# Kernel tuning notes

Measured on AMD Instinct MI355X. Metric: run time of the kernel, lower is better.

## Reference

```python
import jax, jax.numpy as jnp
import numpy as np

EPS = 1e-5
SCALE_MIN, SCALE_MAX = 0.6, 1.0


def _layer_norm(x):
    m = jnp.mean(x, axis=-1, keepdims=True)
    v = jnp.mean((x - m) ** 2, axis=-1, keepdims=True)
    return (x - m) / jnp.sqrt(v + EPS)


def _scan_dir(seq, A, Bp, Cp, D, W_in, W_out, snr_scale):
    """seq: [B, L, C] -> [B, L, C]. Diagonal SSM recurrence h = A*h + B*u."""
    Bsz, L, C = seq.shape
    N = A.shape[0]
    seq = _layer_norm(seq)
    u = jnp.einsum('blc,nc->bln', seq, W_in)                 # input_proj, [B,L,N]
    A_base = jnp.tanh(A)[None, :]                            # [1,N]
    s = jnp.clip(snr_scale, 0.0, 1.0)[:, None]               # [B,1]
    scale = SCALE_MIN + (SCALE_MAX - SCALE_MIN) * s
    Ad = jnp.clip(A_base * scale, -0.99, 0.99)               # [B,N]
    Bu = Bp[None, None, :] * u                               # [B,L,N]

    def step(h, bu_t):
        h = Ad * h + bu_t
        return h, h

    h0 = jnp.zeros((Bsz, N), dtype=seq.dtype)
    _, hs = jax.lax.scan(step, h0, jnp.swapaxes(Bu, 0, 1))   # hs: [L,B,N]
    hs = jnp.swapaxes(hs, 0, 1)                              # [B,L,N]
    y_state = Cp[None, None, :] * hs
    y = jnp.einsum('bln,cn->blc', y_state, W_out)            # output_proj
    return y + D[None, None, :] * seq


def _forward(x, snr_scale, A, Bparam, Cparam, D, W_in, W_out):
    Bsz, H, W, C = x.shape
    L = H * W
    if L > 4000:
        x = _layer_norm(x)
    # row scans
    seq_row = x.reshape(Bsz, L, C)
    y_row_f = _scan_dir(seq_row, A, Bparam, Cparam, D, W_in, W_out, snr_scale)
    y_row_b = _scan_dir(seq_row[:, ::-1, :], A, Bparam, Cparam, D, W_in, W_out, snr_scale)
    y_row = 0.5 * (y_row_f + y_row_b[:, ::-1, :])
    y_row = y_row.reshape(Bsz, H, W, C)
    # column scans
    x_col = jnp.transpose(x, (0, 2, 1, 3))                   # [B,W,H,C]
    seq_col = x_col.reshape(Bsz, L, C)
    y_col_f = _scan_dir(seq_col, A, Bparam, Cparam, D, W_in, W_out, snr_scale)
    y_col_b = _scan_dir(seq_col[:, ::-1, :], A, Bparam, Cparam, D, W_in, W_out, snr_scale)
    y_col = 0.5 * (y_col_f + y_col_b[:, ::-1, :])
    y_col = jnp.transpose(y_col.reshape(Bsz, W, H, C), (0, 2, 1, 3))
    return 0.5 * (y_row + y_col)


def setup_inputs() -> dict:
    key = jax.random.key(0)
    k = jax.random.split(key, 4)
    Bsz, H, W, C, N = 8, 64, 64, 256, 64
    x = jax.random.normal(k[0], (Bsz, H, W, C), dtype=jnp.float32)
    snr_scale = jax.random.uniform(k[1], (Bsz,), dtype=jnp.float32)
    A = -0.5 * jnp.ones((N,), dtype=jnp.float32)
    Bparam = 0.5 * jnp.ones((N,), dtype=jnp.float32)
    Cparam = 0.5 * jnp.ones((N,), dtype=jnp.float32)
    D = jnp.zeros((C,), dtype=jnp.float32)
    # nn.Linear default init: U(-1/sqrt(fan_in), 1/sqrt(fan_in))
    W_in = jax.random.uniform(k[2], (N, C), dtype=jnp.float32,
                              minval=-1.0 / np.sqrt(C), maxval=1.0 / np.sqrt(C))
    W_out = jax.random.uniform(k[3], (C, N), dtype=jnp.float32,
                               minval=-1.0 / np.sqrt(N), maxval=1.0 / np.sqrt(N))
    return {"x": x, "snr_scale": snr_scale, "A": A, "Bparam": Bparam,
            "Cparam": Cparam, "D": D, "W_in": W_in, "W_out": W_out}


def reference(x, snr_scale, A, Bparam, Cparam, D, W_in, W_out):
    return _forward(x, snr_scale, A, Bparam, Cparam, D, W_in, W_out)
```

## Files before the change

kernel.cpp:

```cpp
#include <hip/hip_runtime.h>
#include <hip/hip_bf16.h>
#include <math.h>

#define Bsz 8
#define Hh 64
#define Ww 64
#define Cc 256
#define Nn 64
#define Ll 4096
#define EPSf 1e-5f

typedef __bf16 v8bf __attribute__((ext_vector_type(8)));
typedef float  f32x4 __attribute__((ext_vector_type(4)));

__device__ __forceinline__ float ad_val(float a, float snr) {
    float s = fminf(fmaxf(snr, 0.f), 1.f);
    float scale = 0.6f + 0.4f * s;
    float v = tanhf(a) * scale;
    return fminf(fmaxf(v, -0.99f), 0.99f);
}

__global__ __launch_bounds__(256) void k0_weights(
    const float* __restrict__ Win, const float* __restrict__ Wout,
    const float* __restrict__ Bp, __bf16* __restrict__ Wh,
    __bf16* __restrict__ Wl, __bf16* __restrict__ Wo, float* __restrict__ WB)
{
    const int t = threadIdx.x;
    for (int idx = t; idx < 32 * 64; idx += 256) {
        int tile = idx >> 6, lane = idx & 63;
        int kt = tile >> 2, nt = tile & 3;
        int q = lane >> 4, n = nt * 16 + (lane & 15);
        #pragma unroll
        for (int j = 0; j < 8; ++j) {
            int k = kt * 32 + q * 8 + j;
            float w = Win[n * Cc + k];
            __bf16 h = (__bf16)w;
            Wh[idx * 8 + j] = h;
            Wl[idx * 8 + j] = (__bf16)(w - (float)h);
        }
    }
    for (int idx = t; idx < 32 * 64; idx += 256) {
        int tile = idx >> 6, lane = idx & 63;
        int kt = tile >> 4, ntg = tile & 15;
        int q = lane >> 4, c = ntg * 16 + (lane & 15);
        #pragma unroll
        for (int j = 0; j < 8; ++j) {
            int k = kt * 32 + q * 8 + j;
            Wo[idx * 8 + j] = (__bf16)Wout[c * Nn + k];
        }
    }
    if (t < 64) {
        float s = 0.f;
        for (int c2 = 0; c2 < Cc; ++c2) s += Win[t * Cc + c2];
        WB[t] = s * Bp[t];
    }
}

__global__ __launch_bounds__(256) void k1_ln_gemm(
    const float* __restrict__ x, const __bf16* __restrict__ Wh,
    const __bf16* __restrict__ Wl, const float* __restrict__ Bp,
    const float* __restrict__ WB, float* __restrict__ Bu,
    float* __restrict__ Mst, float* __restrict__ Sst)
{
    __shared__ float mrow[64], srow[64];
    const int t = threadIdx.x;
    const int lane = t & 63;
    const int wv = __builtin_amdgcn_readfirstlane(t >> 6);
    const long pbase = (long)blockIdx.x * 64;
    const float* xt = x + pbase * Cc;

    for (int rr = 0; rr < 16; ++rr) {
        int r = wv * 16 + rr;
        float4 v = ((const float4*)(xt + (long)r * Cc))[lane];
        float s = v.x + v.y + v.z + v.w;
        float q = v.x*v.x + v.y*v.y + v.z*v.z + v.w*v.w;
        #pragma unroll
        for (int off = 32; off > 0; off >>= 1) {
            s += __shfl_down(s, off);
            q += __shfl_down(q, off);
        }
        if (lane == 0) {
            float m = s * (1.f/256.f);
            float var = fmaxf(q * (1.f/256.f) - m*m, 0.f);
            float r1 = rsqrtf(var + EPSf);
            float v2 = var / (var + EPSf);
            float sc = r1 * rsqrtf(v2 + EPSf);
            mrow[r] = m;
            srow[r] = sc;
            Mst[pbase + r] = m;
            Sst[pbase + r] = sc;
        }
    }
    __syncthreads();

    const int q = lane >> 4;
    const int mi = lane & 15;
    const float* xa = xt + (long)(wv * 16 + mi) * Cc + q * 8;

    f32x4 acc[4];
    #pragma unroll
    for (int nt = 0; nt < 4; ++nt) acc[nt] = (f32x4){0.f, 0.f, 0.f, 0.f};

    #pragma unroll
    for (int kt = 0; kt < 8; ++kt) {
        float4 a0 = *(const float4*)(xa + kt * 32);
        float4 a1 = *(const float4*)(xa + kt * 32 + 4);
        float av[8] = {a0.x, a0.y, a0.z, a0.w, a1.x, a1.y, a1.z, a1.w};
        v8bf ah, al;
        #pragma unroll
        for (int j = 0; j < 8; ++j) {
            __bf16 h = (__bf16)av[j];
            ah[j] = h;
            al[j] = (__bf16)(av[j] - (float)h);
        }
        #pragma unroll
        for (int nt = 0; nt < 4; ++nt) {
            v8bf bh = *(const v8bf*)(Wh + ((long)(kt * 4 + nt) * 64 + lane) * 8);
            v8bf bl = *(const v8bf*)(Wl + ((long)(kt * 4 + nt) * 64 + lane) * 8);
            acc[nt] = __builtin_amdgcn_mfma_f32_16x16x32_bf16(ah, bh, acc[nt], 0, 0, 0);
            acc[nt] = __builtin_amdgcn_mfma_f32_16x16x32_bf16(al, bh, acc[nt], 0, 0, 0);
            acc[nt] = __builtin_amdgcn_mfma_f32_16x16x32_bf16(ah, bl, acc[nt], 0, 0, 0);
        }
    }

    #pragma unroll
    for (int nt = 0; nt < 4; ++nt) {
        int n = nt * 16 + mi;
        float bpn = Bp[n];
        float wbn = WB[n];
        #pragma unroll
        for (int reg = 0; reg < 4; ++reg) {
            int p = wv * 16 + q * 4 + reg;
            float m = mrow[p], s = srow[p];
            Bu[(pbase + p) * Nn + n] = s * (acc[nt][reg] * bpn - m * wbn);
        }
    }
}

__global__ __launch_bounds__(64) void k2_carry(
    const float* __restrict__ Bu, const float* __restrict__ A,
    const float* __restrict__ snr, float* __restrict__ E)
{
    __shared__ float tile[64 * 65];
    const int lane = threadIdx.x;
    const int id = blockIdx.x;
    const int isCol = id >> 9;
    const int b = (id >> 6) & 7;
    const int j = id & 63;
    const float Ad = ad_val(A[lane], snr[b]);
    const float* src = Bu + ((long)b * Ll + (isCol ? j : j * 64)) * Nn;
    const long stride = isCol ? (long)Ww * Nn : Nn;
    for (int k = 0; k < 64; ++k)
        tile[k * 65 + lane] = src[k * stride + lane];
    __syncthreads();
    float s = 0.f;
    #pragma unroll 8
    for (int k = 0; k < 64; ++k) s = fmaf(Ad, s, tile[k * 65 + lane]);
    const int dF = isCol ? 2 : 0;
    E[((dF * 8 + b) * 64 + j) * 64 + lane] = s;
    s = 0.f;
    #pragma unroll 8
    for (int k = 63; k >= 0; --k) s = fmaf(Ad, s, tile[k * 65 + lane]);
    E[(((dF + 1) * 8 + b) * 64 + (63 - j)) * 64 + lane] = s;
}

__global__ __launch_bounds__(64) void k3_scan_carries(
    const float* __restrict__ E, float* __restrict__ Hx,
    const float* __restrict__ A, const float* __restrict__ snr)
{
    const int lane = threadIdx.x;
    const int db = blockIdx.x;
    const int b = db & 7;
    float Ad = ad_val(A[lane], snr[b]);
    float p = Ad;
    #pragma unroll
    for (int i = 0; i < 6; ++i) p *= p;
    float s = 0.f;
    const float* e = E + (long)db * 64 * 64;
    float* h = Hx + (long)db * 64 * 64;
    for (int jj = 0; jj < 64; ++jj) {
        h[jj * 64 + lane] = s;
        s = fmaf(p, s, e[jj * 64 + lane]);
    }
}

__global__ __launch_bounds__(64) void k4_apply(
    const float* __restrict__ Bu, const float* __restrict__ Hx,
    const float* __restrict__ A, const float* __restrict__ snr,
    const float* __restrict__ Cp, float* __restrict__ Srow,
    float* __restrict__ Scol)
{
    __shared__ float tile[64 * 65];
    __shared__ float hf[64 * 65];
    const int lane = threadIdx.x;
    const int id = blockIdx.x;
    const int isCol = id >> 9;
    const int b = (id >> 6) & 7;
    const int j = id & 63;
    const float Ad = ad_val(A[lane], snr[b]);
    const float cp = 0.25f * Cp[lane];
    const float* src = Bu + ((long)b * Ll + (isCol ? j : j * 64)) * Nn;
    const long stride = isCol ? (long)Ww * Nn : Nn;
    for (int k = 0; k < 64; ++k)
        tile[k * 65 + lane] = src[k * stride + lane];
    __syncthreads();
    const int dF = isCol ? 2 : 0;
    float s = Hx[((dF * 8 + b) * 64 + j) * 64 + lane];
    for (int k = 0; k < 64; ++k) {
        s = fmaf(Ad, s, tile[k * 65 + lane]);
        hf[k * 65 + lane] = s;
    }
    float sb = Hx[(((dF + 1) * 8 + b) * 64 + (63 - j)) * 64 + lane];
    float* out0 = (isCol ? Scol : Srow) + ((long)b * Ll + (isCol ? j : j * 64)) * Nn;
    for (int k = 63; k >= 0; --k) {
        sb = fmaf(Ad, sb, tile[k * 65 + lane]);
        out0[k * stride + lane] = cp * (sb + hf[k * 65 + lane]);
    }
}

__global__ __launch_bounds__(256) void k5_gemm_out(
    const float* __restrict__ Srow, const float* __restrict__ Scol,
    const float* __restrict__ x, const __bf16* __restrict__ Wo,
    const float* __restrict__ Dp, const float* __restrict__ Mst,
    const float* __restrict__ Sst, float* __restrict__ out)
{
    const int t = threadIdx.x;
    const int lane = t & 63;
    const int wv = __builtin_amdgcn_readfirstlane(t >> 6);
    const int mtile = wv >> 1;
    const int nh = wv & 1;
    const long pbase = (long)blockIdx.x * 32;
    const int q = lane >> 4;
    const int mi = lane & 15;

    const float* sr = Srow + (pbase + mtile * 16 + mi) * Nn + q * 8;
    const float* sc = Scol + (pbase + mtile * 16 + mi) * Nn + q * 8;

    f32x4 acc[8];
    #pragma unroll
    for (int nt = 0; nt < 8; ++nt) acc[nt] = (f32x4){0.f, 0.f, 0.f, 0.f};

    #pragma unroll
    for (int kt = 0; kt < 2; ++kt) {
        float4 r0 = *(const float4*)(sr + kt * 32);
        float4 r1 = *(const float4*)(sr + kt * 32 + 4);
        float4 c0 = *(const float4*)(sc + kt * 32);
        float4 c1 = *(const float4*)(sc + kt * 32 + 4);
        float sv[8] = {r0.x + c0.x, r0.y + c0.y, r0.z + c0.z, r0.w + c0.w,
                       r1.x + c1.x, r1.y + c1.y, r1.z + c1.z, r1.w + c1.w};
        v8bf af;
        #pragma unroll
        for (int j = 0; j < 8; ++j) af[j] = (__bf16)sv[j];
        #pragma unroll
        for (int nt = 0; nt < 8; ++nt) {
            int ntg = nh * 8 + nt;
            v8bf b = *(const v8bf*)(Wo + ((long)(kt * 16 + ntg) * 64 + lane) * 8);
            acc[nt] = __builtin_amdgcn_mfma_f32_16x16x32_bf16(af, b, acc[nt], 0, 0, 0);
        }
    }

    #pragma unroll
    for (int nt = 0; nt < 8; ++nt) {
        int c = nh * 128 + nt * 16 + mi;
        float dc = Dp[c];
        #pragma unroll
        for (int reg = 0; reg < 4; ++reg) {
            long p = pbase + mtile * 16 + q * 4 + reg;
            float m = Mst[p], s = Sst[p];
            long off = p * Cc + c;
            out[off] = acc[nt][reg] + dc * ((x[off] - m) * s);
        }
    }
}

extern "C" void kernel_launch(void* const* d_in, const int* in_sizes, int n_in,
                              void* d_out, int out_size, void* d_ws, size_t ws_size,
                              hipStream_t stream)
{
    const float* x    = (const float*)d_in[0];
    const float* snr  = (const float*)d_in[1];
    const float* A    = (const float*)d_in[2];
    const float* Bp   = (const float*)d_in[3];
    const float* Cp   = (const float*)d_in[4];
    const float* Dp   = (const float*)d_in[5];
    const float* Win  = (const float*)d_in[6];
    const float* Wout = (const float*)d_in[7];
    float* out = (float*)d_out;

    char* ws = (char*)d_ws;
    float*  Bu   = (float*)(ws);
    float*  Srow = (float*)(ws + (size_t)8  * 1024 * 1024);
    float*  Scol = (float*)(ws + (size_t)16 * 1024 * 1024);
    float*  E    = (float*)(ws + (size_t)24 * 1024 * 1024);
    float*  Hx   = (float*)(ws + (size_t)24 * 1024 * 1024 + 512*1024);
    float*  Mst  = (float*)(ws + (size_t)25 * 1024 * 1024);
    float*  Sst  = (float*)(ws + (size_t)25 * 1024 * 1024 + 128*1024);
    char*   wbase = ws + (size_t)25 * 1024 * 1024 + 512 * 1024;
    __bf16* Wh   = (__bf16*)(wbase);
    __bf16* Wl   = (__bf16*)(wbase + 32 * 1024);
    __bf16* Wo   = (__bf16*)(wbase + 64 * 1024);
    float*  WB   = (float*)(wbase + 96 * 1024);

    hipLaunchKernelGGL(k0_weights,      dim3(1),    dim3(256), 0, stream, Win, Wout, Bp, Wh, Wl, Wo, WB);
    hipLaunchKernelGGL(k1_ln_gemm,      dim3(512),  dim3(256), 0, stream, x, Wh, Wl, Bp, WB, Bu, Mst, Sst);
    hipLaunchKernelGGL(k2_carry,        dim3(1024), dim3(64),  0, stream, Bu, A, snr, E);
    hipLaunchKernelGGL(k3_scan_carries, dim3(32),   dim3(64),  0, stream, E, Hx, A, snr);
    hipLaunchKernelGGL(k4_apply,        dim3(1024), dim3(64),  0, stream, Bu, Hx, A, snr, Cp, Srow, Scol);
    hipLaunchKernelGGL(k5_gemm_out,     dim3(1024), dim3(256), 0, stream, Srow, Scol, x, Wo, Dp, Mst, Sst, out);
}
```

Measured before the change: 155.6 us.

## Fuse scan stages into cooperative kernel and stage GEMM tiles through shared memory

```diff
diff --git a/kernel.cpp b/kernel.cpp
--- a/kernel.cpp
+++ b/kernel.cpp
@@ -1,6 +1,9 @@
 #include <hip/hip_runtime.h>
 #include <hip/hip_bf16.h>
+#include <hip/hip_cooperative_groups.h>
 #include <math.h>
+
+namespace cg = cooperative_groups;
 
 #define Bsz 8
 #define Hh 64
@@ -20,39 +23,53 @@
     return fminf(fmaxf(v, -0.99f), 0.99f);
 }
 
+__device__ __forceinline__ v8bf cvt8(float4 a, float4 b) {
+    v8bf r;
+    r[0] = (__bf16)a.x; r[1] = (__bf16)a.y; r[2] = (__bf16)a.z; r[3] = (__bf16)a.w;
+    r[4] = (__bf16)b.x; r[5] = (__bf16)b.y; r[6] = (__bf16)b.z; r[7] = (__bf16)b.w;
+    return r;
+}
+
 __global__ __launch_bounds__(256) void k0_weights(
     const float* __restrict__ Win, const float* __restrict__ Wout,
     const float* __restrict__ Bp, __bf16* __restrict__ Wh,
     __bf16* __restrict__ Wl, __bf16* __restrict__ Wo, float* __restrict__ WB)
 {
     const int t = threadIdx.x;
-    for (int idx = t; idx < 32 * 64; idx += 256) {
-        int tile = idx >> 6, lane = idx & 63;
-        int kt = tile >> 2, nt = tile & 3;
-        int q = lane >> 4, n = nt * 16 + (lane & 15);
-        #pragma unroll
-        for (int j = 0; j < 8; ++j) {
-            int k = kt * 32 + q * 8 + j;
-            float w = Win[n * Cc + k];
-            __bf16 h = (__bf16)w;
-            Wh[idx * 8 + j] = h;
-            Wl[idx * 8 + j] = (__bf16)(w - (float)h);
-        }
-    }
-    for (int idx = t; idx < 32 * 64; idx += 256) {
-        int tile = idx >> 6, lane = idx & 63;
-        int kt = tile >> 4, ntg = tile & 15;
-        int q = lane >> 4, c = ntg * 16 + (lane & 15);
-        #pragma unroll
-        for (int j = 0; j < 8; ++j) {
-            int k = kt * 32 + q * 8 + j;
-            Wo[idx * 8 + j] = (__bf16)Wout[c * Nn + k];
-        }
-    }
-    if (t < 64) {
+    const int blk = blockIdx.x;
+    if (blk < 4) {
+        for (int idx = blk * 512 + t; idx < blk * 512 + 512; idx += 256) {
+            int tile = idx >> 6, lane = idx & 63;
+            int kt = tile >> 2, nt = tile & 3;
+            int q = lane >> 4, n = nt * 16 + (lane & 15);
+            #pragma unroll
+            for (int j = 0; j < 8; ++j) {
+                int k = kt * 32 + q * 8 + j;
+                float w = Win[n * Cc + k];
+                __bf16 h = (__bf16)w;
+                Wh[idx * 8 + j] = h;
+                Wl[idx * 8 + j] = (__bf16)(w - (float)h);
+            }
+        }
+    } else if (blk < 8) {
+        for (int idx = (blk - 4) * 512 + t; idx < (blk - 4) * 512 + 512; idx += 256) {
+            int tile = idx >> 6, lane = idx & 63;
+            int kt = tile >> 4, ntg = tile & 15;
+            int q = lane >> 4, c = ntg * 16 + (lane & 15);
+            #pragma unroll
+            for (int j = 0; j < 8; ++j)
+                Wo[idx * 8 + j] = (__bf16)Wout[c * Nn + kt * 32 + q * 8 + j];
+        }
+    } else {
+        __shared__ float wtmp[256];
+        int n = t >> 2, qd = t & 3;
         float s = 0.f;
-        for (int c2 = 0; c2 < Cc; ++c2) s += Win[t * Cc + c2];
-        WB[t] = s * Bp[t];
+        const float* wr = Win + (long)n * Cc + qd * 64;
+        for (int i = 0; i < 64; ++i) s += wr[i];
+        wtmp[t] = s;
+        __syncthreads();
+        if (t < 64)
+            WB[t] = (wtmp[t*4] + wtmp[t*4+1] + wtmp[t*4+2] + wtmp[t*4+3]) * Bp[t];
     }
 }
 
@@ -62,16 +79,18 @@
     const float* __restrict__ WB, float* __restrict__ Bu,
     float* __restrict__ Mst, float* __restrict__ Sst)
 {
+    __shared__ float xs[64 * 260];
     __shared__ float mrow[64], srow[64];
     const int t = threadIdx.x;
     const int lane = t & 63;
     const int wv = __builtin_amdgcn_readfirstlane(t >> 6);
     const long pbase = (long)blockIdx.x * 64;
-    const float* xt = x + pbase * Cc;
-
-    for (int rr = 0; rr < 16; ++rr) {
-        int r = wv * 16 + rr;
-        float4 v = ((const float4*)(xt + (long)r * Cc))[lane];
+    const float4* xg = (const float4*)(x + pbase * Cc);
+
+    for (int i = 0; i < 16; ++i) {
+        int r = i * 4 + wv;
+        float4 v = xg[i * 256 + t];
+        *(float4*)&xs[r * 260 + lane * 4] = v;
         float s = v.x + v.y + v.z + v.w;
         float q = v.x*v.x + v.y*v.y + v.z*v.z + v.w*v.w;
         #pragma unroll
@@ -85,17 +104,14 @@
             float r1 = rsqrtf(var + EPSf);
             float v2 = var / (var + EPSf);
             float sc = r1 * rsqrtf(v2 + EPSf);
-            mrow[r] = m;
-            srow[r] = sc;
-            Mst[pbase + r] = m;
-            Sst[pbase + r] = sc;
+            mrow[r] = m; srow[r] = sc;
+            Mst[pbase + r] = m; Sst[pbase + r] = sc;
         }
     }
     __syncthreads();
 
     const int q = lane >> 4;
     const int mi = lane & 15;
-    const float* xa = xt + (long)(wv * 16 + mi) * Cc + q * 8;
 
     f32x4 acc[4];
     #pragma unroll
@@ -103,8 +119,9 @@
 
     #pragma unroll
     for (int kt = 0; kt < 8; ++kt) {
-        float4 a0 = *(const float4*)(xa + kt * 32);
-        float4 a1 = *(const float4*)(xa + kt * 32 + 4);
+        const float* ar = &xs[(wv * 16 + mi) * 260 + q * 8 + kt * 32];
+        float4 a0 = *(const float4*)ar;
+        float4 a1 = *(const float4*)(ar + 4);
         float av[8] = {a0.x, a0.y, a0.z, a0.w, a1.x, a1.y, a1.z, a1.w};
         v8bf ah, al;
         #pragma unroll
@@ -123,72 +140,42 @@
         }
     }
 
+    float mv[4], sv[4];
+    #pragma unroll
+    for (int reg = 0; reg < 4; ++reg) {
+        int p = wv * 16 + q * 4 + reg;
+        mv[reg] = mrow[p]; sv[reg] = srow[p];
+    }
+    float buv[4][4];
     #pragma unroll
     for (int nt = 0; nt < 4; ++nt) {
         int n = nt * 16 + mi;
-        float bpn = Bp[n];
-        float wbn = WB[n];
-        #pragma unroll
-        for (int reg = 0; reg < 4; ++reg) {
-            int p = wv * 16 + q * 4 + reg;
-            float m = mrow[p], s = srow[p];
-            Bu[(pbase + p) * Nn + n] = s * (acc[nt][reg] * bpn - m * wbn);
-        }
-    }
-}
-
-__global__ __launch_bounds__(64) void k2_carry(
+        float bpn = Bp[n], wbn = WB[n];
+        #pragma unroll
+        for (int reg = 0; reg < 4; ++reg)
+            buv[nt][reg] = sv[reg] * (acc[nt][reg] * bpn - mv[reg] * wbn);
+    }
+    __syncthreads();
+    #pragma unroll
+    for (int nt = 0; nt < 4; ++nt) {
+        int n = nt * 16 + mi;
+        #pragma unroll
+        for (int reg = 0; reg < 4; ++reg)
+            xs[(wv * 16 + q * 4 + reg) * 68 + n] = buv[nt][reg];
+    }
+    __syncthreads();
+    float4* bug = (float4*)(Bu + pbase * Nn);
+    #pragma unroll
+    for (int i = 0; i < 4; ++i) {
+        int fi = i * 256 + t;
+        bug[fi] = *(const float4*)&xs[(fi >> 4) * 68 + (fi & 15) * 4];
+    }
+}
+
+__global__ __launch_bounds__(64) void k2_scan(
     const float* __restrict__ Bu, const float* __restrict__ A,
-    const float* __restrict__ snr, float* __restrict__ E)
-{
-    __shared__ float tile[64 * 65];
-    const int lane = threadIdx.x;
-    const int id = blockIdx.x;
-    const int isCol = id >> 9;
-    const int b = (id >> 6) & 7;
-    const int j = id & 63;
-    const float Ad = ad_val(A[lane], snr[b]);
-    const float* src = Bu + ((long)b * Ll + (isCol ? j : j * 64)) * Nn;
-    const long stride = isCol ? (long)Ww * Nn : Nn;
-    for (int k = 0; k < 64; ++k)
-        tile[k * 65 + lane] = src[k * stride + lane];
-    __syncthreads();
-    float s = 0.f;
-    #pragma unroll 8
-    for (int k = 0; k < 64; ++k) s = fmaf(Ad, s, tile[k * 65 + lane]);
-    const int dF = isCol ? 2 : 0;
-    E[((dF * 8 + b) * 64 + j) * 64 + lane] = s;
-    s = 0.f;
-    #pragma unroll 8
-    for (int k = 63; k >= 0; --k) s = fmaf(Ad, s, tile[k * 65 + lane]);
-    E[(((dF + 1) * 8 + b) * 64 + (63 - j)) * 64 + lane] = s;
-}
-
-__global__ __launch_bounds__(64) void k3_scan_carries(
-    const float* __restrict__ E, float* __restrict__ Hx,
-    const float* __restrict__ A, const float* __restrict__ snr)
-{
-    const int lane = threadIdx.x;
-    const int db = blockIdx.x;
-    const int b = db & 7;
-    float Ad = ad_val(A[lane], snr[b]);
-    float p = Ad;
-    #pragma unroll
-    for (int i = 0; i < 6; ++i) p *= p;
-    float s = 0.f;
-    const float* e = E + (long)db * 64 * 64;
-    float* h = Hx + (long)db * 64 * 64;
-    for (int jj = 0; jj < 64; ++jj) {
-        h[jj * 64 + lane] = s;
-        s = fmaf(p, s, e[jj * 64 + lane]);
-    }
-}
-
-__global__ __launch_bounds__(64) void k4_apply(
-    const float* __restrict__ Bu, const float* __restrict__ Hx,
-    const float* __restrict__ A, const float* __restrict__ snr,
-    const float* __restrict__ Cp, float* __restrict__ Srow,
-    float* __restrict__ Scol)
+    const float* __restrict__ snr, const float* __restrict__ Cp,
+    float* __restrict__ E, float* __restrict__ Srow, float* __restrict__ Scol)
 {
     __shared__ float tile[64 * 65];
     __shared__ float hf[64 * 65];
@@ -203,18 +190,49 @@
     const long stride = isCol ? (long)Ww * Nn : Nn;
     for (int k = 0; k < 64; ++k)
         tile[k * 65 + lane] = src[k * stride + lane];
-    __syncthreads();
-    const int dF = isCol ? 2 : 0;
-    float s = Hx[((dF * 8 + b) * 64 + j) * 64 + lane];
+
+    float s = 0.f;
+    #pragma unroll 8
     for (int k = 0; k < 64; ++k) {
         s = fmaf(Ad, s, tile[k * 65 + lane]);
         hf[k * 65 + lane] = s;
     }
-    float sb = Hx[(((dF + 1) * 8 + b) * 64 + (63 - j)) * 64 + lane];
-    float* out0 = (isCol ? Scol : Srow) + ((long)b * Ll + (isCol ? j : j * 64)) * Nn;
+    const int dF = isCol ? 2 : 0;
+    E[((dF * 8 + b) * 64 + j) * 64 + lane] = s;
+    float sb = 0.f;
+    #pragma unroll 8
     for (int k = 63; k >= 0; --k) {
         sb = fmaf(Ad, sb, tile[k * 65 + lane]);
-        out0[k * stride + lane] = cp * (sb + hf[k * 65 + lane]);
+        tile[k * 65 + lane] = sb;
+    }
+    E[(((dF + 1) * 8 + b) * 64 + (63 - j)) * 64 + lane] = sb;
+
+    cg::this_grid().sync();
+
+    float p64 = Ad;
+    #pragma unroll
+    for (int i = 0; i < 6; ++i) p64 *= p64;
+    float cf = 0.f;
+    const float* Ef = E + (long)((dF * 8 + b) * 64) * 64;
+    for (int i = 0; i < j; ++i) cf = fmaf(p64, cf, Ef[i * 64 + lane]);
+    float cb = 0.f;
+    const float* Eb = E + (long)(((dF + 1) * 8 + b) * 64) * 64;
+    const int jj = 63 - j;
+    for (int i = 0; i < jj; ++i) cb = fmaf(p64, cb, Eb[i * 64 + lane]);
+
+    float* out0 = (isCol ? Scol : Srow) + ((long)b * Ll + (isCol ? j : j * 64)) * Nn;
+    float pw = Ad;
+    #pragma unroll 8
+    for (int k = 0; k < 64; ++k) {
+        hf[k * 65 + lane] = fmaf(pw, cf, hf[k * 65 + lane]);
+        pw *= Ad;
+    }
+    float pwb = Ad;
+    #pragma unroll 8
+    for (int k = 63; k >= 0; --k) {
+        float val = fmaf(pwb, cb, tile[k * 65 + lane]);
+        out0[k * stride + lane] = cp * (hf[k * 65 + lane] + val);
+        pwb *= Ad;
     }
 }
 
@@ -224,52 +242,72 @@
     const float* __restrict__ Dp, const float* __restrict__ Mst,
     const float* __restrict__ Sst, float* __restrict__ out)
 {
+    __shared__ float smem[64 * 260];
     const int t = threadIdx.x;
     const int lane = t & 63;
     const int wv = __builtin_amdgcn_readfirstlane(t >> 6);
-    const int mtile = wv >> 1;
-    const int nh = wv & 1;
-    const long pbase = (long)blockIdx.x * 32;
+    const long pbase = (long)blockIdx.x * 64;
     const int q = lane >> 4;
     const int mi = lane & 15;
 
-    const float* sr = Srow + (pbase + mtile * 16 + mi) * Nn + q * 8;
-    const float* sc = Scol + (pbase + mtile * 16 + mi) * Nn + q * 8;
-
-    f32x4 acc[8];
-    #pragma unroll
-    for (int nt = 0; nt < 8; ++nt) acc[nt] = (f32x4){0.f, 0.f, 0.f, 0.f};
+    const float4* Sr = (const float4*)(Srow + pbase * Nn);
+    const float4* Sc = (const float4*)(Scol + pbase * Nn);
+    #pragma unroll
+    for (int i = 0; i < 4; ++i) {
+        int fi = i * 256 + t;
+        float4 a = Sr[fi], c = Sc[fi];
+        *(float4*)&smem[(fi >> 4) * 68 + (fi & 15) * 4] =
+            make_float4(a.x + c.x, a.y + c.y, a.z + c.z, a.w + c.w);
+    }
+    __syncthreads();
+
+    f32x4 acc[4][4];
+    #pragma unroll
+    for (int mt = 0; mt < 4; ++mt)
+        #pragma unroll
+        for (int nt = 0; nt < 4; ++nt) acc[mt][nt] = (f32x4){0.f, 0.f, 0.f, 0.f};
 
     #pragma unroll
     for (int kt = 0; kt < 2; ++kt) {
-        float4 r0 = *(const float4*)(sr + kt * 32);
-        float4 r1 = *(const float4*)(sr + kt * 32 + 4);
-        float4 c0 = *(const float4*)(sc + kt * 32);
-        float4 c1 = *(const float4*)(sc + kt * 32 + 4);
-        float sv[8] = {r0.x + c0.x, r0.y + c0.y, r0.z + c0.z, r0.w + c0.w,
-                       r1.x + c1.x, r1.y + c1.y, r1.z + c1.z, r1.w + c1.w};
-        v8bf af;
-        #pragma unroll
-        for (int j = 0; j < 8; ++j) af[j] = (__bf16)sv[j];
-        #pragma unroll
-        for (int nt = 0; nt < 8; ++nt) {
-            int ntg = nh * 8 + nt;
-            v8bf b = *(const v8bf*)(Wo + ((long)(kt * 16 + ntg) * 64 + lane) * 8);
-            acc[nt] = __builtin_amdgcn_mfma_f32_16x16x32_bf16(af, b, acc[nt], 0, 0, 0);
-        }
-    }
-
-    #pragma unroll
-    for (int nt = 0; nt < 8; ++nt) {
-        int c = nh * 128 + nt * 16 + mi;
-        float dc = Dp[c];
-        #pragma unroll
-        for (int reg = 0; reg < 4; ++reg) {
-            long p = pbase + mtile * 16 + q * 4 + reg;
-            float m = Mst[p], s = Sst[p];
-            long off = p * Cc + c;
-            out[off] = acc[nt][reg] + dc * ((x[off] - m) * s);
-        }
+        v8bf bfr[4];
+        #pragma unroll
+        for (int nt = 0; nt < 4; ++nt)
+            bfr[nt] = *(const v8bf*)(Wo + ((long)(kt * 16 + wv * 4 + nt) * 64 + lane) * 8);
+        #pragma unroll
+        for (int mt = 0; mt < 4; ++mt) {
+            const float* ar = &smem[(mt * 16 + mi) * 68 + q * 8 + kt * 32];
+            v8bf af = cvt8(*(const float4*)ar, *(const float4*)(ar + 4));
+            #pragma unroll
+            for (int nt = 0; nt < 4; ++nt)
+                acc[mt][nt] = __builtin_amdgcn_mfma_f32_16x16x32_bf16(af, bfr[nt], acc[mt][nt], 0, 0, 0);
+        }
+    }
+    __syncthreads();
+    #pragma unroll
+    for (int mt = 0; mt < 4; ++mt)
+        #pragma unroll
+        for (int nt = 0; nt < 4; ++nt) {
+            int c = wv * 64 + nt * 16 + mi;
+            #pragma unroll
+            for (int reg = 0; reg < 4; ++reg)
+                smem[(mt * 16 + q * 4 + reg) * 260 + c] = acc[mt][nt][reg];
+        }
+    __syncthreads();
+
+    const float4* xg = (const float4*)(x + pbase * Cc);
+    float4* og = (float4*)(out + pbase * Cc);
+    const float4 dv = ((const float4*)Dp)[lane];
+    #pragma unroll 4
+    for (int i = 0; i < 16; ++i) {
+        int fi = i * 256 + t;
+        int p = i * 4 + wv;
+        float4 v = *(const float4*)&smem[p * 260 + lane * 4];
+        float m = Mst[pbase + p], s = Sst[pbase + p];
+        float4 xv = xg[fi];
+        og[fi] = make_float4(v.x + dv.x * ((xv.x - m) * s),
+                             v.y + dv.y * ((xv.y - m) * s),
+                             v.z + dv.z * ((xv.z - m) * s),
+                             v.w + dv.w * ((xv.w - m) * s));
     }
 }
 
@@ -292,7 +330,6 @@
     float*  Srow = (float*)(ws + (size_t)8  * 1024 * 1024);
     float*  Scol = (float*)(ws + (size_t)16 * 1024 * 1024);
     float*  E    = (float*)(ws + (size_t)24 * 1024 * 1024);
-    float*  Hx   = (float*)(ws + (size_t)24 * 1024 * 1024 + 512*1024);
     float*  Mst  = (float*)(ws + (size_t)25 * 1024 * 1024);
     float*  Sst  = (float*)(ws + (size_t)25 * 1024 * 1024 + 128*1024);
     char*   wbase = ws + (size_t)25 * 1024 * 1024 + 512 * 1024;
@@ -301,10 +338,12 @@
     __bf16* Wo   = (__bf16*)(wbase + 64 * 1024);
     float*  WB   = (float*)(wbase + 96 * 1024);
 
-    hipLaunchKernelGGL(k0_weights,      dim3(1),    dim3(256), 0, stream, Win, Wout, Bp, Wh, Wl, Wo, WB);
-    hipLaunchKernelGGL(k1_ln_gemm,      dim3(512),  dim3(256), 0, stream, x, Wh, Wl, Bp, WB, Bu, Mst, Sst);
-    hipLaunchKernelGGL(k2_carry,        dim3(1024), dim3(64),  0, stream, Bu, A, snr, E);
-    hipLaunchKernelGGL(k3_scan_carries, dim3(32),   dim3(64),  0, stream, E, Hx, A, snr);
-    hipLaunchKernelGGL(k4_apply,        dim3(1024), dim3(64),  0, stream, Bu, Hx, A, snr, Cp, Srow, Scol);
-    hipLaunchKernelGGL(k5_gemm_out,     dim3(1024), dim3(256), 0, stream, Srow, Scol, x, Wo, Dp, Mst, Sst, out);
-}
+    hipLaunchKernelGGL(k0_weights, dim3(9),   dim3(256), 0, stream, Win, Wout, Bp, Wh, Wl, Wo, WB);
+    hipLaunchKernelGGL(k1_ln_gemm, dim3(512), dim3(256), 0, stream, x, Wh, Wl, Bp, WB, Bu, Mst, Sst);
+
+    void* args[] = {(void*)&Bu, (void*)&A, (void*)&snr, (void*)&Cp,
+                    (void*)&E, (void*)&Srow, (void*)&Scol};
+    hipLaunchCooperativeKernel((void*)k2_scan, dim3(1024), dim3(64), args, 0, stream);
+
+    hipLaunchKernelGGL(k5_gemm_out, dim3(512), dim3(256), 0, stream, Srow, Scol, x, Wo, Dp, Mst, Sst, out);
+}
```

Result: slower. 208.9 us (+34.3%).
